# Kernel optimization log

Hardware: AMD Instinct MI355X
Metric: run time of the kernel (lower is better)

The kernel has to match this reference:

```python
import jax, jax.numpy as jnp
import numpy as np

B, H, L, D = 8, 4, 1024, 64

def setup_inputs() -> dict:
    key = jax.random.key(0)
    ks = jax.random.split(key, 6)
    s = 1.0 / np.sqrt(D)
    return {
        "X": jax.random.normal(ks[0], (B, H, L, D), dtype=jnp.float32),
        "Y": jax.random.normal(ks[1], (B, H, L, D), dtype=jnp.float32),
        "W1": jax.random.normal(ks[2], (D, D), dtype=jnp.float32) * s,
        "b1": jax.random.normal(ks[3], (D,), dtype=jnp.float32) * s,
        "w2": jax.random.normal(ks[4], (D,), dtype=jnp.float32) * s,
        "b2": jax.random.normal(ks[5], (), dtype=jnp.float32) * s,
    }

def reference(X, Y, W1, b1, w2, b2):
    # Original: net[b,i,j,d] = (lin1(X))[b,d,i]*(lin1(Y))[b,d,j]; out = relu(net @ w2 + b2)
    # Algebraically: out[b,i,j] = relu(sum_d w2[d]*Xf[b,i,d]*Yf[b,j,d] + b2)
    Bx, Hx, Lx, Dx = X.shape
    Xf = X.reshape(-1, Lx, Dx) @ W1.T + b1   # [B*H, L, D]
    Yf = Y.reshape(-1, Lx, Dx) @ W1.T + b1   # [B*H, L, D]
    scores = jnp.einsum('bid,bjd->bij', Xf * w2, Yf) + b2  # [B*H, L, L]
    out = jax.nn.relu(scores)
    return out.reshape(Bx, -1, Lx, Lx)
```

## Files before the change

kernel.cpp:

```cpp
#include <hip/hip_runtime.h>

#define BH 32
#define L  1024
#define D  64

typedef short  short8  __attribute__((ext_vector_type(8)));
typedef __bf16 bf16x8  __attribute__((ext_vector_type(8)));
typedef float  f32x16  __attribute__((ext_vector_type(16)));

__device__ __forceinline__ unsigned short f2bf(float f) {
    union { float f; unsigned u; } v; v.f = f;
    unsigned r = v.u + 0x7fffu + ((v.u >> 16) & 1u);
    return (unsigned short)(r >> 16);
}

__global__ __launch_bounds__(256, 4) void proj_kernel(
    const float* __restrict__ X, const float* __restrict__ Y,
    const float* __restrict__ W1, const float* __restrict__ b1,
    const float* __restrict__ w2,
    unsigned short* __restrict__ Xs, unsigned short* __restrict__ Yf)
{
    __shared__ unsigned short Wl[64 * 72];
    __shared__ unsigned short Al[128 * 72];

    const int tid = threadIdx.x;
    const bool isX = (blockIdx.y == 0);
    const float* src = isX ? X : Y;
    unsigned short* dst = isX ? Xs : Yf;
    const int r0 = blockIdx.x * 128;

    {
        const int d  = tid >> 2;
        const int kb = (tid & 3) * 16;
        const float4* wp = (const float4*)(W1 + d * 64 + kb);
        #pragma unroll
        for (int q = 0; q < 4; ++q) {
            float4 v = wp[q];
            unsigned short* o = &Wl[d * 72 + kb + q * 4];
            o[0] = f2bf(v.x); o[1] = f2bf(v.y); o[2] = f2bf(v.z); o[3] = f2bf(v.w);
        }
    }
    {
        const float4* xp = (const float4*)(src + (size_t)r0 * 64);
        #pragma unroll
        for (int p = 0; p < 8; ++p) {
            int c = tid + 256 * p;
            float4 v = xp[c];
            int row = c >> 4;
            int c4  = (c & 15) * 4;
            unsigned short* o = &Al[row * 72 + c4];
            o[0] = f2bf(v.x); o[1] = f2bf(v.y); o[2] = f2bf(v.z); o[3] = f2bf(v.w);
        }
    }
    __syncthreads();

    const int w   = tid >> 6;
    const int l   = tid & 63;
    const int l31 = l & 31;
    const int lh  = l >> 5;

    f32x16 acc[2] = {};

    const int arow = w * 32 + l31;
    #pragma unroll
    for (int kk = 0; kk < 4; ++kk) {
        int k0 = kk * 16 + lh * 8;
        bf16x8 a = *(const bf16x8*)&Al[arow * 72 + k0];
        #pragma unroll
        for (int nt = 0; nt < 2; ++nt) {
            bf16x8 b = *(const bf16x8*)&Wl[(nt * 32 + l31) * 72 + k0];
            acc[nt] = __builtin_amdgcn_mfma_f32_32x32x16_bf16(a, b, acc[nt], 0, 0, 0);
        }
    }

    #pragma unroll
    for (int nt = 0; nt < 2; ++nt) {
        int d = nt * 32 + l31;
        float bb = b1[d];
        float ww = isX ? w2[d] : 1.0f;
        #pragma unroll
        for (int r = 0; r < 16; ++r) {
            int row = w * 32 + 4 * lh + (r & 3) + 8 * (r >> 2);
            float v = (acc[nt][r] + bb) * ww;
            dst[(size_t)(r0 + row) * 64 + d] = f2bf(v);
        }
    }
}

__global__ __launch_bounds__(256, 4) void score_kernel(
    const unsigned short* __restrict__ Xs, const unsigned short* __restrict__ Yf,
    const float* __restrict__ b2p, float* __restrict__ out)
{
    __shared__ unsigned short As[128 * 72];
    __shared__ unsigned short Bs[128 * 72];

    const int tid = threadIdx.x;
    const int bh  = blockIdx.z;
    const int i0  = blockIdx.y * 128;
    const int j0  = blockIdx.x * 128;

    const unsigned short* aSrc = Xs + ((size_t)bh * L + i0) * D;
    const unsigned short* bSrc = Yf + ((size_t)bh * L + j0) * D;

    #pragma unroll
    for (int p = 0; p < 4; ++p) {
        int c   = tid + 256 * p;
        int row = c >> 3;
        int col = c & 7;
        short8 va = *(const short8*)(aSrc + (size_t)c * 8);
        short8 vb = *(const short8*)(bSrc + (size_t)c * 8);
        *(short8*)&As[row * 72 + col * 8] = va;
        *(short8*)&Bs[row * 72 + col * 8] = vb;
    }
    __syncthreads();

    const int w    = tid >> 6;
    const int l    = tid & 63;
    const int l31  = l & 31;
    const int lh   = l >> 5;
    const int wrow = (w >> 1) * 64;
    const int wcol = (w & 1) * 64;

    f32x16 acc[2][2] = {};

    #pragma unroll
    for (int kk = 0; kk < 4; ++kk) {
        int k0 = kk * 16 + lh * 8;
        bf16x8 a0 = *(const bf16x8*)&As[(wrow +      l31) * 72 + k0];
        bf16x8 a1 = *(const bf16x8*)&As[(wrow + 32 + l31) * 72 + k0];
        bf16x8 b0 = *(const bf16x8*)&Bs[(wcol +      l31) * 72 + k0];
        bf16x8 b1 = *(const bf16x8*)&Bs[(wcol + 32 + l31) * 72 + k0];
        acc[0][0] = __builtin_amdgcn_mfma_f32_32x32x16_bf16(a0, b0, acc[0][0], 0, 0, 0);
        acc[0][1] = __builtin_amdgcn_mfma_f32_32x32x16_bf16(a0, b1, acc[0][1], 0, 0, 0);
        acc[1][0] = __builtin_amdgcn_mfma_f32_32x32x16_bf16(a1, b0, acc[1][0], 0, 0, 0);
        acc[1][1] = __builtin_amdgcn_mfma_f32_32x32x16_bf16(a1, b1, acc[1][1], 0, 0, 0);
    }

    const float b2 = b2p[0];
    float* obase = out + (size_t)bh * L * L;

    #pragma unroll
    for (int ti = 0; ti < 2; ++ti) {
        #pragma unroll
        for (int tj = 0; tj < 2; ++tj) {
            int gj = j0 + wcol + tj * 32 + l31;
            #pragma unroll
            for (int r = 0; r < 16; ++r) {
                int gi = i0 + wrow + ti * 32 + 4 * lh + (r & 3) + 8 * (r >> 2);
                float v = acc[ti][tj][r] + b2;
                v = v > 0.0f ? v : 0.0f;
                obase[(size_t)gi * L + gj] = v;
            }
        }
    }
}

extern "C" void kernel_launch(void* const* d_in, const int* in_sizes, int n_in,
                              void* d_out, int out_size, void* d_ws, size_t ws_size,
                              hipStream_t stream) {
    (void)in_sizes; (void)n_in; (void)out_size; (void)ws_size;
    const float* X  = (const float*)d_in[0];
    const float* Y  = (const float*)d_in[1];
    const float* W1 = (const float*)d_in[2];
    const float* b1 = (const float*)d_in[3];
    const float* w2 = (const float*)d_in[4];
    const float* b2 = (const float*)d_in[5];
    float* out = (float*)d_out;

    unsigned short* Xs = (unsigned short*)d_ws;
    unsigned short* Yf = Xs + (size_t)BH * L * D;

    dim3 pgrid(256, 2, 1);
    proj_kernel<<<pgrid, 256, 0, stream>>>(X, Y, W1, b1, w2, Xs, Yf);

    dim3 ggrid(8, 8, BH);
    score_kernel<<<ggrid, 256, 0, stream>>>(Xs, Yf, b2, out);
}
```

Before: 161.2 us.

## Fuse projection into score kernel, recomputing projected tiles per block

Merges the projection and score kernels into one launch. Each score block now loads its raw fp32 X and Y tiles, projects them with W1 using MFMA, and writes the results into shared memory before running the score GEMM. This removes the second launch and the workspace write and read round trip. In exchange every X and Y row is reprojected 8 times across blocks, the blocks read fp32 inputs instead of bf16, shared memory and register use grow, and launch bounds drop to 3 blocks per SM.

Measured after the change: 170.9 us. +6.0%, slower.

```diff
diff --git a/kernel.cpp b/kernel.cpp
--- a/kernel.cpp
+++ b/kernel.cpp
@@ -3,8 +3,8 @@
 #define BH 32
 #define L  1024
 #define D  64
+#define PAD 72
 
-typedef short  short8  __attribute__((ext_vector_type(8)));
 typedef __bf16 bf16x8  __attribute__((ext_vector_type(8)));
 typedef float  f32x16  __attribute__((ext_vector_type(16)));
 
@@ -14,20 +14,20 @@
     return (unsigned short)(r >> 16);
 }
 
-__global__ __launch_bounds__(256, 4) void proj_kernel(
+__global__ __launch_bounds__(256, 3) void fused_kernel(
     const float* __restrict__ X, const float* __restrict__ Y,
     const float* __restrict__ W1, const float* __restrict__ b1,
-    const float* __restrict__ w2,
-    unsigned short* __restrict__ Xs, unsigned short* __restrict__ Yf)
+    const float* __restrict__ w2, const float* __restrict__ b2p,
+    float* __restrict__ out)
 {
-    __shared__ unsigned short Wl[64 * 72];
-    __shared__ unsigned short Al[128 * 72];
+    __shared__ unsigned short Wl[64 * PAD];
+    __shared__ unsigned short As[128 * PAD];
+    __shared__ unsigned short Bs[128 * PAD];
 
     const int tid = threadIdx.x;
-    const bool isX = (blockIdx.y == 0);
-    const float* src = isX ? X : Y;
-    unsigned short* dst = isX ? Xs : Yf;
-    const int r0 = blockIdx.x * 128;
+    const int bh  = blockIdx.z;
+    const int i0  = blockIdx.y * 128;
+    const int j0  = blockIdx.x * 128;
 
     {
         const int d  = tid >> 2;
@@ -36,20 +36,24 @@
         #pragma unroll
         for (int q = 0; q < 4; ++q) {
             float4 v = wp[q];
-            unsigned short* o = &Wl[d * 72 + kb + q * 4];
+            unsigned short* o = &Wl[d * PAD + kb + q * 4];
             o[0] = f2bf(v.x); o[1] = f2bf(v.y); o[2] = f2bf(v.z); o[3] = f2bf(v.w);
         }
     }
     {
-        const float4* xp = (const float4*)(src + (size_t)r0 * 64);
+        const float4* xp = (const float4*)(X + ((size_t)bh * L + i0) * D);
+        const float4* yp = (const float4*)(Y + ((size_t)bh * L + j0) * D);
         #pragma unroll
         for (int p = 0; p < 8; ++p) {
-            int c = tid + 256 * p;
-            float4 v = xp[c];
+            int c   = tid + 256 * p;
             int row = c >> 4;
             int c4  = (c & 15) * 4;
-            unsigned short* o = &Al[row * 72 + c4];
-            o[0] = f2bf(v.x); o[1] = f2bf(v.y); o[2] = f2bf(v.z); o[3] = f2bf(v.w);
+            float4 vx = xp[c];
+            float4 vy = yp[c];
+            unsigned short* ox = &As[row * PAD + c4];
+            ox[0] = f2bf(vx.x); ox[1] = f2bf(vx.y); ox[2] = f2bf(vx.z); ox[3] = f2bf(vx.w);
+            unsigned short* oy = &Bs[row * PAD + c4];
+            oy[0] = f2bf(vy.x); oy[1] = f2bf(vy.y); oy[2] = f2bf(vy.z); oy[3] = f2bf(vy.w);
         }
     }
     __syncthreads();
@@ -59,65 +63,42 @@
     const int l31 = l & 31;
     const int lh  = l >> 5;
 
-    f32x16 acc[2] = {};
-
-    const int arow = w * 32 + l31;
-    #pragma unroll
-    for (int kk = 0; kk < 4; ++kk) {
-        int k0 = kk * 16 + lh * 8;
-        bf16x8 a = *(const bf16x8*)&Al[arow * 72 + k0];
+    {
+        const int arow = w * 32 + l31;
+        bf16x8 ax[4], ay[4];
+        #pragma unroll
+        for (int kk = 0; kk < 4; ++kk) {
+            int k0 = kk * 16 + lh * 8;
+            ax[kk] = *(const bf16x8*)&As[arow * PAD + k0];
+            ay[kk] = *(const bf16x8*)&Bs[arow * PAD + k0];
+        }
+        f32x16 accx[2] = {};
+        f32x16 accy[2] = {};
+        #pragma unroll
+        for (int kk = 0; kk < 4; ++kk) {
+            int k0 = kk * 16 + lh * 8;
+            #pragma unroll
+            for (int nt = 0; nt < 2; ++nt) {
+                bf16x8 wv = *(const bf16x8*)&Wl[(nt * 32 + l31) * PAD + k0];
+                accx[nt] = __builtin_amdgcn_mfma_f32_32x32x16_bf16(ax[kk], wv, accx[nt], 0, 0, 0);
+                accy[nt] = __builtin_amdgcn_mfma_f32_32x32x16_bf16(ay[kk], wv, accy[nt], 0, 0, 0);
+            }
+        }
         #pragma unroll
         for (int nt = 0; nt < 2; ++nt) {
-            bf16x8 b = *(const bf16x8*)&Wl[(nt * 32 + l31) * 72 + k0];
-            acc[nt] = __builtin_amdgcn_mfma_f32_32x32x16_bf16(a, b, acc[nt], 0, 0, 0);
+            int d = nt * 32 + l31;
+            float bb  = b1[d];
+            float wwx = w2[d];
+            #pragma unroll
+            for (int r = 0; r < 16; ++r) {
+                int row = w * 32 + 4 * lh + (r & 3) + 8 * (r >> 2);
+                As[row * PAD + d] = f2bf((accx[nt][r] + bb) * wwx);
+                Bs[row * PAD + d] = f2bf(accy[nt][r] + bb);
+            }
         }
-    }
-
-    #pragma unroll
-    for (int nt = 0; nt < 2; ++nt) {
-        int d = nt * 32 + l31;
-        float bb = b1[d];
-        float ww = isX ? w2[d] : 1.0f;
-        #pragma unroll
-        for (int r = 0; r < 16; ++r) {
-            int row = w * 32 + 4 * lh + (r & 3) + 8 * (r >> 2);
-            float v = (acc[nt][r] + bb) * ww;
-            dst[(size_t)(r0 + row) * 64 + d] = f2bf(v);
-        }
-    }
-}
-
-__global__ __launch_bounds__(256, 4) void score_kernel(
-    const unsigned short* __restrict__ Xs, const unsigned short* __restrict__ Yf,
-    const float* __restrict__ b2p, float* __restrict__ out)
-{
-    __shared__ unsigned short As[128 * 72];
-    __shared__ unsigned short Bs[128 * 72];
-
-    const int tid = threadIdx.x;
-    const int bh  = blockIdx.z;
-    const int i0  = blockIdx.y * 128;
-    const int j0  = blockIdx.x * 128;
-
-    const unsigned short* aSrc = Xs + ((size_t)bh * L + i0) * D;
-    const unsigned short* bSrc = Yf + ((size_t)bh * L + j0) * D;
-
-    #pragma unroll
-    for (int p = 0; p < 4; ++p) {
-        int c   = tid + 256 * p;
-        int row = c >> 3;
-        int col = c & 7;
-        short8 va = *(const short8*)(aSrc + (size_t)c * 8);
-        short8 vb = *(const short8*)(bSrc + (size_t)c * 8);
-        *(short8*)&As[row * 72 + col * 8] = va;
-        *(short8*)&Bs[row * 72 + col * 8] = vb;
     }
     __syncthreads();
 
-    const int w    = tid >> 6;
-    const int l    = tid & 63;
-    const int l31  = l & 31;
-    const int lh   = l >> 5;
     const int wrow = (w >> 1) * 64;
     const int wcol = (w & 1) * 64;
 
@@ -126,14 +107,14 @@
     #pragma unroll
     for (int kk = 0; kk < 4; ++kk) {
         int k0 = kk * 16 + lh * 8;
-        bf16x8 a0 = *(const bf16x8*)&As[(wrow +      l31) * 72 + k0];
-        bf16x8 a1 = *(const bf16x8*)&As[(wrow + 32 + l31) * 72 + k0];
-        bf16x8 b0 = *(const bf16x8*)&Bs[(wcol +      l31) * 72 + k0];
-        bf16x8 b1 = *(const bf16x8*)&Bs[(wcol + 32 + l31) * 72 + k0];
-        acc[0][0] = __builtin_amdgcn_mfma_f32_32x32x16_bf16(a0, b0, acc[0][0], 0, 0, 0);
-        acc[0][1] = __builtin_amdgcn_mfma_f32_32x32x16_bf16(a0, b1, acc[0][1], 0, 0, 0);
-        acc[1][0] = __builtin_amdgcn_mfma_f32_32x32x16_bf16(a1, b0, acc[1][0], 0, 0, 0);
-        acc[1][1] = __builtin_amdgcn_mfma_f32_32x32x16_bf16(a1, b1, acc[1][1], 0, 0, 0);
+        bf16x8 a0 = *(const bf16x8*)&As[(wrow +      l31) * PAD + k0];
+        bf16x8 a1 = *(const bf16x8*)&As[(wrow + 32 + l31) * PAD + k0];
+        bf16x8 b0 = *(const bf16x8*)&Bs[(wcol +      l31) * PAD + k0];
+        bf16x8 b1v = *(const bf16x8*)&Bs[(wcol + 32 + l31) * PAD + k0];
+        acc[0][0] = __builtin_amdgcn_mfma_f32_32x32x16_bf16(a0, b0,  acc[0][0], 0, 0, 0);
+        acc[0][1] = __builtin_amdgcn_mfma_f32_32x32x16_bf16(a0, b1v, acc[0][1], 0, 0, 0);
+        acc[1][0] = __builtin_amdgcn_mfma_f32_32x32x16_bf16(a1, b0,  acc[1][0], 0, 0, 0);
+        acc[1][1] = __builtin_amdgcn_mfma_f32_32x32x16_bf16(a1, b1v, acc[1][1], 0, 0, 0);
     }
 
     const float b2 = b2p[0];
@@ -158,7 +139,7 @@
 extern "C" void kernel_launch(void* const* d_in, const int* in_sizes, int n_in,
                               void* d_out, int out_size, void* d_ws, size_t ws_size,
                               hipStream_t stream) {
-    (void)in_sizes; (void)n_in; (void)out_size; (void)ws_size;
+    (void)in_sizes; (void)n_in; (void)out_size; (void)d_ws; (void)ws_size;
     const float* X  = (const float*)d_in[0];
     const float* Y  = (const float*)d_in[1];
     const float* W1 = (const float*)d_in[2];
@@ -167,12 +148,6 @@
     const float* b2 = (const float*)d_in[5];
     float* out = (float*)d_out;
 
-    unsigned short* Xs = (unsigned short*)d_ws;
-    unsigned short* Yf = Xs + (size_t)BH * L * D;
-
-    dim3 pgrid(256, 2, 1);
-    proj_kernel<<<pgrid, 256, 0, stream>>>(X, Y, W1, b1, w2, Xs, Yf);
-
-    dim3 ggrid(8, 8, BH);
-    score_kernel<<<ggrid, 256, 0, stream>>>(Xs, Yf, b2, out);
+    dim3 grid(8, 8, BH);
+    fused_kernel<<<grid, 256, 0, stream>>>(X, Y, W1, b1, w2, b2, out);
 }
```

## Widen score tiles to full row strips with swizzled shared Y panel

Applied to the files above, without the earlier changes.

The score kernel now uses 512-thread blocks that each cover a 128-row strip across all 1024 columns. The whole per-head Y panel (128 KB) sits in LDS with an XOR swizzle to avoid bank conflicts, and each wave computes 2x4 MFMA tiles per pass. This reloads X/Y tiles far less often and gives larger contiguous output row writes. The projection kernel also switches its bf16 LDS stores from scalar to 4-wide vectors. The trade-off is 128 KB+ of LDS per block, which limits occupancy to about one block per CU, and a grid of only 256 blocks.

Result: slower. 164.6 us (+2.1%).

```diff
diff --git a/kernel.cpp b/kernel.cpp
--- a/kernel.cpp
+++ b/kernel.cpp
@@ -7,6 +7,7 @@
 typedef short  short8  __attribute__((ext_vector_type(8)));
 typedef __bf16 bf16x8  __attribute__((ext_vector_type(8)));
 typedef float  f32x16  __attribute__((ext_vector_type(16)));
+typedef unsigned short us4 __attribute__((ext_vector_type(4)));
 
 __device__ __forceinline__ unsigned short f2bf(float f) {
     union { float f; unsigned u; } v; v.f = f;
@@ -36,8 +37,8 @@
         #pragma unroll
         for (int q = 0; q < 4; ++q) {
             float4 v = wp[q];
-            unsigned short* o = &Wl[d * 72 + kb + q * 4];
-            o[0] = f2bf(v.x); o[1] = f2bf(v.y); o[2] = f2bf(v.z); o[3] = f2bf(v.w);
+            us4 t = { f2bf(v.x), f2bf(v.y), f2bf(v.z), f2bf(v.w) };
+            *(us4*)&Wl[d * 72 + kb + q * 4] = t;
         }
     }
     {
@@ -48,8 +49,8 @@
             float4 v = xp[c];
             int row = c >> 4;
             int c4  = (c & 15) * 4;
-            unsigned short* o = &Al[row * 72 + c4];
-            o[0] = f2bf(v.x); o[1] = f2bf(v.y); o[2] = f2bf(v.z); o[3] = f2bf(v.w);
+            us4 t = { f2bf(v.x), f2bf(v.y), f2bf(v.z), f2bf(v.w) };
+            *(us4*)&Al[row * 72 + c4] = t;
         }
     }
     __syncthreads();
@@ -87,69 +88,79 @@
     }
 }
 
-__global__ __launch_bounds__(256, 4) void score_kernel(
+__global__ __launch_bounds__(512, 2) void score_kernel(
     const unsigned short* __restrict__ Xs, const unsigned short* __restrict__ Yf,
     const float* __restrict__ b2p, float* __restrict__ out)
 {
     __shared__ unsigned short As[128 * 72];
-    __shared__ unsigned short Bs[128 * 72];
+    __shared__ unsigned short Bs[1024 * 64];
 
     const int tid = threadIdx.x;
-    const int bh  = blockIdx.z;
+    const int bh  = blockIdx.x;
     const int i0  = blockIdx.y * 128;
-    const int j0  = blockIdx.x * 128;
 
     const unsigned short* aSrc = Xs + ((size_t)bh * L + i0) * D;
-    const unsigned short* bSrc = Yf + ((size_t)bh * L + j0) * D;
+    const unsigned short* bSrc = Yf + (size_t)bh * L * D;
 
     #pragma unroll
-    for (int p = 0; p < 4; ++p) {
-        int c   = tid + 256 * p;
+    for (int p = 0; p < 2; ++p) {
+        int c   = tid + 512 * p;
         int row = c >> 3;
-        int col = c & 7;
-        short8 va = *(const short8*)(aSrc + (size_t)c * 8);
-        short8 vb = *(const short8*)(bSrc + (size_t)c * 8);
-        *(short8*)&As[row * 72 + col * 8] = va;
-        *(short8*)&Bs[row * 72 + col * 8] = vb;
+        int sl  = c & 7;
+        *(short8*)&As[row * 72 + sl * 8] = *(const short8*)(aSrc + (size_t)c * 8);
+    }
+    #pragma unroll
+    for (int p = 0; p < 16; ++p) {
+        int c   = tid + 512 * p;
+        int row = c >> 3;
+        int sl  = (c & 7) ^ (row & 7);
+        *(short8*)&Bs[row * 64 + sl * 8] = *(const short8*)(bSrc + (size_t)c * 8);
     }
     __syncthreads();
 
-    const int w    = tid >> 6;
-    const int l    = tid & 63;
-    const int l31  = l & 31;
-    const int lh   = l >> 5;
-    const int wrow = (w >> 1) * 64;
-    const int wcol = (w & 1) * 64;
+    const int w   = tid >> 6;
+    const int l   = tid & 63;
+    const int l31 = l & 31;
+    const int lh  = l >> 5;
+    const int wr  = w & 1;
+    const int wc  = w >> 1;
 
-    f32x16 acc[2][2] = {};
+    const float b2 = b2p[0];
+    float* obase = out + ((size_t)bh * L + i0) * L;
+    const int xsl = l31 & 7;
 
     #pragma unroll
-    for (int kk = 0; kk < 4; ++kk) {
-        int k0 = kk * 16 + lh * 8;
-        bf16x8 a0 = *(const bf16x8*)&As[(wrow +      l31) * 72 + k0];
-        bf16x8 a1 = *(const bf16x8*)&As[(wrow + 32 + l31) * 72 + k0];
-        bf16x8 b0 = *(const bf16x8*)&Bs[(wcol +      l31) * 72 + k0];
-        bf16x8 b1 = *(const bf16x8*)&Bs[(wcol + 32 + l31) * 72 + k0];
-        acc[0][0] = __builtin_amdgcn_mfma_f32_32x32x16_bf16(a0, b0, acc[0][0], 0, 0, 0);
-        acc[0][1] = __builtin_amdgcn_mfma_f32_32x32x16_bf16(a0, b1, acc[0][1], 0, 0, 0);
-        acc[1][0] = __builtin_amdgcn_mfma_f32_32x32x16_bf16(a1, b0, acc[1][0], 0, 0, 0);
-        acc[1][1] = __builtin_amdgcn_mfma_f32_32x32x16_bf16(a1, b1, acc[1][1], 0, 0, 0);
-    }
+    for (int cc = 0; cc < 2; ++cc) {
+        f32x16 acc[2][4] = {};
+        const int jbase = wc * 256 + cc * 128;
 
-    const float b2 = b2p[0];
-    float* obase = out + (size_t)bh * L * L;
+        #pragma unroll
+        for (int kk = 0; kk < 4; ++kk) {
+            int k0 = kk * 16 + lh * 8;
+            bf16x8 a0 = *(const bf16x8*)&As[(wr * 64 +      l31) * 72 + k0];
+            bf16x8 a1 = *(const bf16x8*)&As[(wr * 64 + 32 + l31) * 72 + k0];
+            int slot = kk * 2 + lh;
+            #pragma unroll
+            for (int tj = 0; tj < 4; ++tj) {
+                int j = jbase + tj * 32 + l31;
+                bf16x8 b = *(const bf16x8*)&Bs[j * 64 + ((slot ^ xsl) * 8)];
+                acc[0][tj] = __builtin_amdgcn_mfma_f32_32x32x16_bf16(a0, b, acc[0][tj], 0, 0, 0);
+                acc[1][tj] = __builtin_amdgcn_mfma_f32_32x32x16_bf16(a1, b, acc[1][tj], 0, 0, 0);
+            }
+        }
 
-    #pragma unroll
-    for (int ti = 0; ti < 2; ++ti) {
         #pragma unroll
-        for (int tj = 0; tj < 2; ++tj) {
-            int gj = j0 + wcol + tj * 32 + l31;
+        for (int si = 0; si < 2; ++si) {
             #pragma unroll
             for (int r = 0; r < 16; ++r) {
-                int gi = i0 + wrow + ti * 32 + 4 * lh + (r & 3) + 8 * (r >> 2);
-                float v = acc[ti][tj][r] + b2;
-                v = v > 0.0f ? v : 0.0f;
-                obase[(size_t)gi * L + gj] = v;
+                int gi = wr * 64 + si * 32 + 4 * lh + (r & 3) + 8 * (r >> 2);
+                float* rowp = obase + (size_t)gi * L + jbase + l31;
+                #pragma unroll
+                for (int tj = 0; tj < 4; ++tj) {
+                    float v = acc[si][tj][r] + b2;
+                    v = v > 0.0f ? v : 0.0f;
+                    rowp[tj * 32] = v;
+                }
             }
         }
     }
@@ -173,6 +184,6 @@
     dim3 pgrid(256, 2, 1);
     proj_kernel<<<pgrid, 256, 0, stream>>>(X, Y, W1, b1, w2, Xs, Yf);
 
-    dim3 ggrid(8, 8, BH);
-    score_kernel<<<ggrid, 256, 0, stream>>>(Xs, Yf, b2, out);
+    dim3 sgrid(32, 8, 1);
+    score_kernel<<<sgrid, 512, 0, stream>>>(Xs, Yf, b2, out);
 }
```

## Stage score tile through LDS for coalesced float4 output stores

Applied to the files above, without the earlier changes.

The score kernel now writes each 32-row chunk of its ReLU'd accumulator tile into shared memory, which reuses the A tile's storage. The whole block then streams that chunk to global memory with row-contiguous float4 stores, replacing the scattered per-lane scalar stores. The goal is wider, fully coalesced writes for the large fp32 output. The price is extra barriers, LDS round trips and some LDS bank conflicts. The projection kernel also packs its bf16 conversions into 4-wide vector LDS stores.

New measurement: 163.3 us. No clear change (+1.3%).

```diff
diff --git a/kernel.cpp b/kernel.cpp
--- a/kernel.cpp
+++ b/kernel.cpp
@@ -7,6 +7,7 @@
 typedef short  short8  __attribute__((ext_vector_type(8)));
 typedef __bf16 bf16x8  __attribute__((ext_vector_type(8)));
 typedef float  f32x16  __attribute__((ext_vector_type(16)));
+typedef unsigned short us4 __attribute__((ext_vector_type(4)));
 
 __device__ __forceinline__ unsigned short f2bf(float f) {
     union { float f; unsigned u; } v; v.f = f;
@@ -36,8 +37,8 @@
         #pragma unroll
         for (int q = 0; q < 4; ++q) {
             float4 v = wp[q];
-            unsigned short* o = &Wl[d * 72 + kb + q * 4];
-            o[0] = f2bf(v.x); o[1] = f2bf(v.y); o[2] = f2bf(v.z); o[3] = f2bf(v.w);
+            us4 t = { f2bf(v.x), f2bf(v.y), f2bf(v.z), f2bf(v.w) };
+            *(us4*)&Wl[d * 72 + kb + q * 4] = t;
         }
     }
     {
@@ -48,8 +49,8 @@
             float4 v = xp[c];
             int row = c >> 4;
             int c4  = (c & 15) * 4;
-            unsigned short* o = &Al[row * 72 + c4];
-            o[0] = f2bf(v.x); o[1] = f2bf(v.y); o[2] = f2bf(v.z); o[3] = f2bf(v.w);
+            us4 t = { f2bf(v.x), f2bf(v.y), f2bf(v.z), f2bf(v.w) };
+            *(us4*)&Al[row * 72 + c4] = t;
         }
     }
     __syncthreads();
@@ -91,7 +92,7 @@
     const unsigned short* __restrict__ Xs, const unsigned short* __restrict__ Yf,
     const float* __restrict__ b2p, float* __restrict__ out)
 {
-    __shared__ unsigned short As[128 * 72];
+    __shared__ alignas(16) unsigned short As[128 * 72];
     __shared__ unsigned short Bs[128 * 72];
 
     const int tid = threadIdx.x;
@@ -129,29 +130,47 @@
         bf16x8 a0 = *(const bf16x8*)&As[(wrow +      l31) * 72 + k0];
         bf16x8 a1 = *(const bf16x8*)&As[(wrow + 32 + l31) * 72 + k0];
         bf16x8 b0 = *(const bf16x8*)&Bs[(wcol +      l31) * 72 + k0];
-        bf16x8 b1 = *(const bf16x8*)&Bs[(wcol + 32 + l31) * 72 + k0];
-        acc[0][0] = __builtin_amdgcn_mfma_f32_32x32x16_bf16(a0, b0, acc[0][0], 0, 0, 0);
-        acc[0][1] = __builtin_amdgcn_mfma_f32_32x32x16_bf16(a0, b1, acc[0][1], 0, 0, 0);
-        acc[1][0] = __builtin_amdgcn_mfma_f32_32x32x16_bf16(a1, b0, acc[1][0], 0, 0, 0);
-        acc[1][1] = __builtin_amdgcn_mfma_f32_32x32x16_bf16(a1, b1, acc[1][1], 0, 0, 0);
+        bf16x8 b1v = *(const bf16x8*)&Bs[(wcol + 32 + l31) * 72 + k0];
+        acc[0][0] = __builtin_amdgcn_mfma_f32_32x32x16_bf16(a0, b0,  acc[0][0], 0, 0, 0);
+        acc[0][1] = __builtin_amdgcn_mfma_f32_32x32x16_bf16(a0, b1v, acc[0][1], 0, 0, 0);
+        acc[1][0] = __builtin_amdgcn_mfma_f32_32x32x16_bf16(a1, b0,  acc[1][0], 0, 0, 0);
+        acc[1][1] = __builtin_amdgcn_mfma_f32_32x32x16_bf16(a1, b1v, acc[1][1], 0, 0, 0);
     }
 
+    __syncthreads();
+
     const float b2 = b2p[0];
-    float* obase = out + (size_t)bh * L * L;
+    float* obase = out + ((size_t)bh * L + i0) * L + j0;
+    float* stage = (float*)As;
 
     #pragma unroll
-    for (int ti = 0; ti < 2; ++ti) {
-        #pragma unroll
-        for (int tj = 0; tj < 2; ++tj) {
-            int gj = j0 + wcol + tj * 32 + l31;
+    for (int chunk = 0; chunk < 4; ++chunk) {
+        if ((w >> 1) == (chunk >> 1)) {
+            const int ti = chunk & 1;
             #pragma unroll
-            for (int r = 0; r < 16; ++r) {
-                int gi = i0 + wrow + ti * 32 + 4 * lh + (r & 3) + 8 * (r >> 2);
-                float v = acc[ti][tj][r] + b2;
-                v = v > 0.0f ? v : 0.0f;
-                obase[(size_t)gi * L + gj] = v;
+            for (int tj = 0; tj < 2; ++tj) {
+                #pragma unroll
+                for (int r = 0; r < 16; ++r) {
+                    int lr = 4 * lh + (r & 3) + 8 * (r >> 2);
+                    int lc = wcol + tj * 32 + l31;
+                    float v = acc[ti][tj][r] + b2;
+                    v = v > 0.0f ? v : 0.0f;
+                    stage[lr * 128 + lc] = v;
+                }
             }
         }
+        __syncthreads();
+        const float4* sp = (const float4*)stage;
+        const int rbase = chunk * 32;
+        #pragma unroll
+        for (int q = 0; q < 4; ++q) {
+            int idx  = tid + 256 * q;
+            float4 v = sp[idx];
+            int lrow = rbase + (idx >> 5);
+            int lcol = (idx & 31) << 2;
+            *(float4*)&obase[(size_t)lrow * L + lcol] = v;
+        }
+        __syncthreads();
     }
 }
 
```
